# Performance work log

Hardware: AMD Instinct MI355X
Metric: run time of the kernel (lower is better)

Reference implementation:

```python
import jax, jax.numpy as jnp
import numpy as np

B, L, M, H = 4096, 512, 17, 17  # batch, seq_len, num_features, latent_dim


def setup_inputs() -> dict:
    key = jax.random.key(0)
    ks = jax.random.split(key, 5)
    s = 1.0 / np.sqrt(H)  # torch nn.LSTM init scale
    x = jax.random.normal(ks[0], (B, L, M), dtype=jnp.float32)
    W_ih = jax.random.uniform(ks[1], (4 * H, M), dtype=jnp.float32, minval=-s, maxval=s)
    W_hh = jax.random.uniform(ks[2], (4 * H, H), dtype=jnp.float32, minval=-s, maxval=s)
    b_ih = jax.random.uniform(ks[3], (4 * H,), dtype=jnp.float32, minval=-s, maxval=s)
    b_hh = jax.random.uniform(ks[4], (4 * H,), dtype=jnp.float32, minval=-s, maxval=s)
    return {"x": x, "W_ih": W_ih, "W_hh": W_hh, "b_ih": b_ih, "b_hh": b_hh}


def _lstm(x, W_ih, W_hh, b_ih, b_hh):
    # Precompute input projections for all timesteps in one GEMM: (B,L,4H)
    xW = jnp.einsum('blm,gm->blg', x, W_ih) + b_ih + b_hh
    xW_t = jnp.swapaxes(xW, 0, 1)  # (L,B,4H) for scan over time
    W_hh_T = W_hh.T  # (H,4H)

    def step(carry, xw_t):
        h, c = carry
        gates = xw_t + h @ W_hh_T  # (B,4H)
        i, f, g, o = jnp.split(gates, 4, axis=-1)  # torch gate order: i,f,g,o
        i = jax.nn.sigmoid(i)
        f = jax.nn.sigmoid(f)
        g = jnp.tanh(g)
        o = jax.nn.sigmoid(o)
        c_new = f * c + i * g
        h_new = o * jnp.tanh(c_new)
        return (h_new, c_new), h_new

    h0 = jnp.zeros((x.shape[0], W_hh.shape[1]), dtype=x.dtype)
    c0 = jnp.zeros_like(h0)
    (h_f, c_f), hs = jax.lax.scan(step, (h0, c0), xW_t)
    out = jnp.swapaxes(hs, 0, 1)  # (B,L,H)
    return out, h_f, c_f


def reference(x, W_ih, W_hh, b_ih, b_hh):
    out, h_f, c_f = _lstm(x, W_ih, W_hh, b_ih, b_hh)
    # match torch return: out, (h,c) with leading num_layers dim, and x
    return out, (h_f[None], c_f[None]), x
```

## Files before the change

kernel.cpp:

```cpp
#include <hip/hip_runtime.h>
#include <hip/hip_bf16.h>


namespace {
constexpr int B_TOT = 4096;
constexpr int L_SEQ = 512;
constexpr int NF    = 17;
constexpr int BS    = 16;
constexpr int TPB   = 320;
constexpr int TC    = 32;
constexpr int NCHUNK = L_SEQ / TC;
constexpr int KPAD  = 24;
constexpr int F4_PER_ROW   = TC * NF / 4;
constexpr int F4_PER_CHUNK = BS * F4_PER_ROW;
constexpr int PF_MAX = (F4_PER_CHUNK + TPB - 1) / TPB;

constexpr int OUT_H = B_TOT * L_SEQ * NF;
constexpr int OUT_C = OUT_H + B_TOT * NF;
constexpr int OUT_X = OUT_C + B_TOT * NF;
}

typedef __attribute__((ext_vector_type(8))) short bf16x8;
typedef __attribute__((ext_vector_type(4))) float f32x4;

__device__ __forceinline__ unsigned short f2bf(float f) {
  union { float f; unsigned int u; } v; v.f = f;
  unsigned int r = v.u + 0x7fff + ((v.u >> 16) & 1);
  return (unsigned short)(r >> 16);
}
__device__ __forceinline__ float sigm(float x) {
  return __builtin_amdgcn_rcpf(1.f + __expf(-x));
}
__device__ __forceinline__ float tanh_fast(float x) {
  float e = __expf(2.f * x);
  return 1.f - 2.f * __builtin_amdgcn_rcpf(e + 1.f);
}

__global__ void __launch_bounds__(TPB) lstm_kernel(
    const float* __restrict__ x, const float* __restrict__ W_ih,
    const float* __restrict__ W_hh, const float* __restrict__ b_ih,
    const float* __restrict__ b_hh, float* __restrict__ out)
{
  __shared__ __align__(16) unsigned short x_s[2][TC][BS][KPAD];
  __shared__ __align__(16) unsigned short h_s[2][BS][KPAD];
  __shared__ __align__(16) unsigned short w0_s[80][32];
  __shared__ __align__(16) unsigned short w1_s[80][32];
  __shared__ __align__(16) float bias_s[80];
  __shared__ __align__(16) unsigned short zero16[8];

  const int tid  = threadIdx.x;
  const int lane = tid & 63;
  const int T    = tid >> 6;
  const int bb   = lane & 15;
  const int q    = lane >> 4;
  const int b0   = blockIdx.x * BS;

  f32x4 pf[PF_MAX];
  #pragma unroll
  for (int i = 0; i < PF_MAX; ++i) {
    int u = tid + TPB * i;
    if (u < F4_PER_CHUNK) {
      int row = u / F4_PER_ROW, off = u % F4_PER_ROW;
      pf[i] = *(const f32x4*)(x + ((b0 + row) * L_SEQ) * NF + off * 4);
    }
  }

  {
    unsigned int* p = (unsigned int*)&x_s[0][0][0][0];
    for (int u = tid; u < (int)(sizeof(x_s) / 4); u += TPB) p[u] = 0;
    unsigned int* ph = (unsigned int*)&h_s[0][0][0];
    for (int u = tid; u < (int)(sizeof(h_s) / 4); u += TPB) ph[u] = 0;
    if (tid < 4) ((unsigned int*)zero16)[tid] = 0;
  }
  for (int u = tid; u < 80 * 32; u += TPB) {
    int r = u >> 5, k = u & 31;
    unsigned short v0 = 0, v1 = 0;
    int j = -1, ty = 0;
    if (r < 64)      { j = r >> 2; ty = r & 3; }
    else if (r < 68) { j = 16;     ty = r - 64; }
    if (j >= 0 && k < NF) {
      int g = ty * NF + j;
      v0 = f2bf(W_ih[g * NF + k]);
      v1 = f2bf(W_hh[g * NF + k]);
    }
    w0_s[r][k] = v0; w1_s[r][k] = v1;
  }
  for (int u = tid; u < 80; u += TPB) {
    float bv = 0.f; int j = -1, ty = 0;
    if (u < 64)      { j = u >> 2; ty = u & 3; }
    else if (u < 68) { j = 16;     ty = u - 64; }
    if (j >= 0) { int g = ty * NF + j; bv = b_ih[g] + b_hh[g]; }
    bias_s[u] = bv;
  }
  __syncthreads();

  auto stage = [&](int cn) {
    #pragma unroll
    for (int i = 0; i < PF_MAX; ++i) {
      int u = tid + TPB * i;
      if (u < F4_PER_CHUNK) {
        int row = u / F4_PER_ROW, off = u % F4_PER_ROW;
        int gidx = ((b0 + row) * L_SEQ + cn * TC) * NF + off * 4;
        *(f32x4*)(out + OUT_X + gidx) = pf[i];
        int p = off * 4, tl = p / NF, m = p - tl * NF;
        #pragma unroll
        for (int e = 0; e < 4; ++e) {
          x_s[cn & 1][tl][row][m] = f2bf(pf[i][e]);
          if (++m == NF) { m = 0; ++tl; }
        }
      }
    }
  };
  auto prefetch = [&](int cn) {
    #pragma unroll
    for (int i = 0; i < PF_MAX; ++i) {
      int u = tid + TPB * i;
      if (u < F4_PER_CHUNK) {
        int row = u / F4_PER_ROW, off = u % F4_PER_ROW;
        pf[i] = *(const f32x4*)(x + ((b0 + row) * L_SEQ + cn * TC) * NF + off * 4);
      }
    }
  };

  stage(0);
  prefetch(1);

  const bf16x8 a0 = *(const bf16x8*)&w0_s[16 * T + bb][q * 8];
  const bf16x8 a1 = *(const bf16x8*)&w1_s[16 * T + bb][q * 8];
  const f32x4 bias4 = *(const f32x4*)&bias_s[16 * T + q * 4];

  const int j = 4 * T + q;
  const bool active = (T < 4) || (q == 0);
  const int jj = (j > 16) ? 16 : j;

  const unsigned short* xbuf[2] = {
    (q == 3) ? zero16 : &x_s[0][0][bb][q * 8],
    (q == 3) ? zero16 : &x_s[1][0][bb][q * 8] };
  const int xstep = (q == 3) ? 0 : BS * KPAD;
  const unsigned short* hr[2] = {
    (q == 3) ? zero16 : &h_s[0][bb][q * 8],
    (q == 3) ? zero16 : &h_s[1][bb][q * 8] };
  unsigned short* hw[2] = { &h_s[1][bb][jj], &h_s[0][bb][jj] };

  float c_st = 0.f, h_last = 0.f;
  float* outp = out + (b0 + bb) * L_SEQ * NF + jj;

  for (int c = 0; c < NCHUNK; ++c) {
    const unsigned short* xp = xbuf[c & 1];
    for (int tt = 0; tt < TC; ++tt) {
      const int t = c * TC + tt;
      __syncthreads();
      bf16x8 bx = *(const bf16x8*)xp;
      bf16x8 bh = *(const bf16x8*)hr[t & 1];
      xp += xstep;
      f32x4 acc = __builtin_amdgcn_mfma_f32_16x16x32_bf16(a0, bx, bias4, 0, 0, 0);
      acc       = __builtin_amdgcn_mfma_f32_16x16x32_bf16(a1, bh, acc,   0, 0, 0);
      if (active) {
        float gi = sigm(acc[0]);
        float gf = sigm(acc[1]);
        float gg = tanh_fast(acc[2]);
        float go = sigm(acc[3]);
        c_st  = gf * c_st + gi * gg;
        h_last = go * tanh_fast(c_st);
        *hw[t & 1] = f2bf(h_last);
        outp[0] = h_last;
        outp += NF;
      }
    }
    if (c + 1 < NCHUNK) {
      stage(c + 1);
      if (c + 2 < NCHUNK) prefetch(c + 2);
    }
  }

  if (active) {
    out[OUT_H + (b0 + bb) * NF + j] = h_last;
    out[OUT_C + (b0 + bb) * NF + j] = c_st;
  }
}

extern "C" void kernel_launch(void* const* d_in, const int* in_sizes, int n_in,
                              void* d_out, int out_size, void* d_ws, size_t ws_size,
                              hipStream_t stream) {
  (void)in_sizes; (void)n_in; (void)out_size; (void)d_ws; (void)ws_size;
  const float* x    = (const float*)d_in[0];
  const float* W_ih = (const float*)d_in[1];
  const float* W_hh = (const float*)d_in[2];
  const float* b_ih = (const float*)d_in[3];
  const float* b_hh = (const float*)d_in[4];
  float* out = (float*)d_out;
  hipLaunchKernelGGL(lstm_kernel, dim3(B_TOT / BS), dim3(TPB), 0, stream,
                     x, W_ih, W_hh, b_ih, b_hh, out);
}
```

Baseline: 497.8 us.

## Rewrite LSTM kernel with 4 waves, register weights and per-step x staging

Cuts the block from 5 to 4 wavefronts: wave 3 computes the extra 17th hidden unit with a second pair of MFMAs. Weights and biases are loaded straight into registers instead of going through shared memory. x is streamed per timestep by wave 0 through a 4-slot register ring and a small LDS ring, replacing the chunked 32-step staging. The h buffer uses a padded, swizzled layout to avoid bank conflicts, and the barrier is a hand-written lgkmcnt wait plus s_barrier. This aims to shorten each serial step's barrier and LDS latency, but wave 3 now does twice the work and wave 0 takes on the global loads, which may make them the critical path.

```diff
diff --git a/kernel.cpp b/kernel.cpp
--- a/kernel.cpp
+++ b/kernel.cpp
@@ -1,181 +1,184 @@
 #include <hip/hip_runtime.h>
-#include <hip/hip_bf16.h>
+#include <string.h>
 
 
+typedef __attribute__((ext_vector_type(8))) short bf16x8;
+typedef __attribute__((ext_vector_type(4))) float f32x4;
+typedef __attribute__((ext_vector_type(4))) int i32x4;
+
 namespace {
-constexpr int B_TOT = 4096;
-constexpr int L_SEQ = 512;
-constexpr int NF    = 17;
-constexpr int BS    = 16;
-constexpr int TPB   = 320;
-constexpr int TC    = 32;
-constexpr int NCHUNK = L_SEQ / TC;
-constexpr int KPAD  = 24;
-constexpr int F4_PER_ROW   = TC * NF / 4;
-constexpr int F4_PER_CHUNK = BS * F4_PER_ROW;
-constexpr int PF_MAX = (F4_PER_CHUNK + TPB - 1) / TPB;
-
+constexpr int B_TOT = 4096, L_SEQ = 512, NF = 17;
 constexpr int OUT_H = B_TOT * L_SEQ * NF;
 constexpr int OUT_C = OUT_H + B_TOT * NF;
 constexpr int OUT_X = OUT_C + B_TOT * NF;
 }
 
-typedef __attribute__((ext_vector_type(8))) short bf16x8;
-typedef __attribute__((ext_vector_type(4))) float f32x4;
-
-__device__ __forceinline__ unsigned short f2bf(float f) {
-  union { float f; unsigned int u; } v; v.f = f;
-  unsigned int r = v.u + 0x7fff + ((v.u >> 16) & 1);
-  return (unsigned short)(r >> 16);
+__device__ __forceinline__ float sigm(float v) {
+  return __builtin_amdgcn_rcpf(1.f + __expf(-v));
 }
-__device__ __forceinline__ float sigm(float x) {
-  return __builtin_amdgcn_rcpf(1.f + __expf(-x));
-}
-__device__ __forceinline__ float tanh_fast(float x) {
-  float e = __expf(2.f * x);
+__device__ __forceinline__ float tanh_f(float v) {
+  float e = __expf(2.f * v);
   return 1.f - 2.f * __builtin_amdgcn_rcpf(e + 1.f);
 }
+__device__ __forceinline__ unsigned pack_bf(float a, float b) {
+  return ((__float_as_uint(a) + 0x8000u) >> 16) | ((__float_as_uint(b) + 0x8000u) & 0xffff0000u);
+}
+__device__ __forceinline__ unsigned short bf1(float a) {
+  return (unsigned short)((__float_as_uint(a) + 0x8000u) >> 16);
+}
 
-__global__ void __launch_bounds__(TPB) lstm_kernel(
+__global__ void __launch_bounds__(256) lstm_kernel(
     const float* __restrict__ x, const float* __restrict__ W_ih,
     const float* __restrict__ W_hh, const float* __restrict__ b_ih,
     const float* __restrict__ b_hh, float* __restrict__ out)
 {
-  __shared__ __align__(16) unsigned short x_s[2][TC][BS][KPAD];
-  __shared__ __align__(16) unsigned short h_s[2][BS][KPAD];
-  __shared__ __align__(16) unsigned short w0_s[80][32];
-  __shared__ __align__(16) unsigned short w1_s[80][32];
-  __shared__ __align__(16) float bias_s[80];
-  __shared__ __align__(16) unsigned short zero16[8];
+  __shared__ unsigned hx[2][4][65];
+  __shared__ unsigned xs[4][4][64];
 
   const int tid  = threadIdx.x;
   const int lane = tid & 63;
-  const int T    = tid >> 6;
+  const int w    = tid >> 6;
   const int bb   = lane & 15;
   const int q    = lane >> 4;
-  const int b0   = blockIdx.x * BS;
+  const int b0   = blockIdx.x * 16;
 
-  f32x4 pf[PF_MAX];
+  for (int u = tid; u < 2 * 4 * 65; u += 256) ((unsigned*)hx)[u] = 0;
+
+  bf16x8 a0[2], a1[2]; f32x4 bias[2];
   #pragma unroll
-  for (int i = 0; i < PF_MAX; ++i) {
-    int u = tid + TPB * i;
-    if (u < F4_PER_CHUNK) {
-      int row = u / F4_PER_ROW, off = u % F4_PER_ROW;
-      pf[i] = *(const f32x4*)(x + ((b0 + row) * L_SEQ) * NF + off * 4);
+  for (int tt = 0; tt < 2; ++tt) {
+    const int T = tt ? 4 : w;
+    unsigned d0[4], d1[4];
+    const int R = 16 * T + bb, j = R >> 2, ty = R & 3;
+    const bool vr = (j <= 16);
+    #pragma unroll
+    for (int u = 0; u < 4; ++u) {
+      const int k0 = 8 * q + u, k1 = k0 + 4;
+      float wa0 = (vr && k0 < NF) ? W_ih[(ty * NF + j) * NF + k0] : 0.f;
+      float wa1 = (vr && k1 < NF) ? W_ih[(ty * NF + j) * NF + k1] : 0.f;
+      float wb0 = (vr && k0 < NF) ? W_hh[(ty * NF + j) * NF + k0] : 0.f;
+      float wb1 = (vr && k1 < NF) ? W_hh[(ty * NF + j) * NF + k1] : 0.f;
+      d0[u] = pack_bf(wa0, wa1);
+      d1[u] = pack_bf(wb0, wb1);
+    }
+    a0[tt] = __builtin_bit_cast(bf16x8, i32x4{(int)d0[0], (int)d0[1], (int)d0[2], (int)d0[3]});
+    a1[tt] = __builtin_bit_cast(bf16x8, i32x4{(int)d1[0], (int)d1[1], (int)d1[2], (int)d1[3]});
+    f32x4 bv;
+    #pragma unroll
+    for (int r = 0; r < 4; ++r) {
+      const int Rc = 16 * T + 4 * q + r, jc = Rc >> 2, tyc = Rc & 3;
+      bv[r] = (jc <= 16) ? (b_ih[tyc * NF + jc] + b_hh[tyc * NF + jc]) : 0.f;
+    }
+    bias[tt] = bv;
+  }
+
+  float xb[4][8];
+  const int xoff = (b0 + bb) * L_SEQ * NF + 8 * q;
+
+  auto load_x = [&](int slot, int t) {
+    const float* p = x + xoff + t * NF;
+    if (q < 2) {
+      memcpy(&xb[slot][0], p, 16);
+      memcpy(&xb[slot][4], p + 4, 16);
+    } else if (q == 2) {
+      xb[slot][0] = p[0];
+      #pragma unroll
+      for (int e = 1; e < 8; ++e) xb[slot][e] = 0.f;
+    } else {
+      #pragma unroll
+      for (int e = 0; e < 8; ++e) xb[slot][e] = 0.f;
+    }
+  };
+  auto stage_x = [&](int t, int slot) {
+    #pragma unroll
+    for (int d = 0; d < 4; ++d)
+      xs[t & 3][d][lane] = pack_bf(xb[slot][d], xb[slot][d + 4]);
+    float* po = out + OUT_X + xoff + t * NF;
+    if (q < 2) {
+      memcpy(po, &xb[slot][0], 16);
+      memcpy(po + 4, &xb[slot][4], 16);
+    } else if (q == 2) {
+      po[0] = xb[slot][0];
+    }
+  };
+
+  if (w == 0) {
+    #pragma unroll
+    for (int k = 0; k < 4; ++k) load_x(k, k);
+    stage_x(0, 0);
+  }
+  __syncthreads();
+
+  unsigned short* hw0[2]; unsigned short* hw1[2];
+  const unsigned* hr[2];
+  #pragma unroll
+  for (int bf = 0; bf < 2; ++bf) {
+    unsigned* p0 = &((unsigned*)hx)[bf * 260 + q * 65 + bb * 4 + (((w >> 1) + bb) & 3)];
+    hw0[bf] = (unsigned short*)p0 + (w & 1);
+    unsigned* p1 = &((unsigned*)hx)[bf * 260 + bb * 4 + ((2 + bb) & 3)];
+    hw1[bf] = (unsigned short*)p1;
+    hr[bf] = &((unsigned*)hx)[bf * 260 + bb * 4 + ((q + bb) & 3)];
+  }
+
+  float c0 = 0.f, c1 = 0.f, hA = 0.f, hB = 0.f;
+  float* op0 = out + (b0 + bb) * L_SEQ * NF + (4 * w + q);
+  float* op1 = out + (b0 + bb) * L_SEQ * NF + 16;
+
+  for (int tb = 0; tb < L_SEQ; tb += 4) {
+    #pragma unroll
+    for (int k = 0; k < 4; ++k) {
+      const int t = tb + k;
+      unsigned bhd[4], bxd[4];
+      const unsigned* hrb = hr[t & 1];
+      #pragma unroll
+      for (int u = 0; u < 4; ++u) bhd[u] = hrb[u * 65];
+      #pragma unroll
+      for (int d = 0; d < 4; ++d) bxd[d] = ((const unsigned*)xs)[(t & 3) * 256 + d * 64 + lane];
+      bf16x8 bh = __builtin_bit_cast(bf16x8, i32x4{(int)bhd[0], (int)bhd[1], (int)bhd[2], (int)bhd[3]});
+      bf16x8 bx = __builtin_bit_cast(bf16x8, i32x4{(int)bxd[0], (int)bxd[1], (int)bxd[2], (int)bxd[3]});
+
+      f32x4 acc0 = __builtin_amdgcn_mfma_f32_16x16x32_bf16(a0[0], bx, bias[0], 0, 0, 0);
+      acc0       = __builtin_amdgcn_mfma_f32_16x16x32_bf16(a1[0], bh, acc0,    0, 0, 0);
+      f32x4 acc1;
+      if (w == 3) {
+        acc1 = __builtin_amdgcn_mfma_f32_16x16x32_bf16(a0[1], bx, bias[1], 0, 0, 0);
+        acc1 = __builtin_amdgcn_mfma_f32_16x16x32_bf16(a1[1], bh, acc1,    0, 0, 0);
+      }
+
+      {
+        float gi = sigm(acc0[0]), gf = sigm(acc0[1]);
+        float gg = tanh_f(acc0[2]), go = sigm(acc0[3]);
+        c0 = gf * c0 + gi * gg;
+        hA = go * tanh_f(c0);
+        *hw0[(t + 1) & 1] = bf1(hA);
+        op0[t * NF] = hA;
+      }
+      if (w == 3) {
+        float gi = sigm(acc1[0]), gf = sigm(acc1[1]);
+        float gg = tanh_f(acc1[2]), go = sigm(acc1[3]);
+        c1 = gf * c1 + gi * gg;
+        hB = go * tanh_f(c1);
+        if (q == 0) {
+          *hw1[(t + 1) & 1] = bf1(hB);
+          op1[t * NF] = hB;
+        }
+      }
+      if (w == 0) {
+        if (t + 1 < L_SEQ) stage_x(t + 1, (t + 1) & 3);
+        if (t + 4 < L_SEQ) load_x(t & 3, t + 4);
+      }
+      asm volatile("s_waitcnt lgkmcnt(0)\n\ts_barrier" ::: "memory");
     }
   }
 
   {
-    unsigned int* p = (unsigned int*)&x_s[0][0][0][0];
-    for (int u = tid; u < (int)(sizeof(x_s) / 4); u += TPB) p[u] = 0;
-    unsigned int* ph = (unsigned int*)&h_s[0][0][0];
-    for (int u = tid; u < (int)(sizeof(h_s) / 4); u += TPB) ph[u] = 0;
-    if (tid < 4) ((unsigned int*)zero16)[tid] = 0;
-  }
-  for (int u = tid; u < 80 * 32; u += TPB) {
-    int r = u >> 5, k = u & 31;
-    unsigned short v0 = 0, v1 = 0;
-    int j = -1, ty = 0;
-    if (r < 64)      { j = r >> 2; ty = r & 3; }
-    else if (r < 68) { j = 16;     ty = r - 64; }
-    if (j >= 0 && k < NF) {
-      int g = ty * NF + j;
-      v0 = f2bf(W_ih[g * NF + k]);
-      v1 = f2bf(W_hh[g * NF + k]);
+    const int jf = 4 * w + q;
+    out[OUT_H + (b0 + bb) * NF + jf] = hA;
+    out[OUT_C + (b0 + bb) * NF + jf] = c0;
+    if (w == 3 && q == 0) {
+      out[OUT_H + (b0 + bb) * NF + 16] = hB;
+      out[OUT_C + (b0 + bb) * NF + 16] = c1;
     }
-    w0_s[r][k] = v0; w1_s[r][k] = v1;
-  }
-  for (int u = tid; u < 80; u += TPB) {
-    float bv = 0.f; int j = -1, ty = 0;
-    if (u < 64)      { j = u >> 2; ty = u & 3; }
-    else if (u < 68) { j = 16;     ty = u - 64; }
-    if (j >= 0) { int g = ty * NF + j; bv = b_ih[g] + b_hh[g]; }
-    bias_s[u] = bv;
-  }
-  __syncthreads();
-
-  auto stage = [&](int cn) {
-    #pragma unroll
-    for (int i = 0; i < PF_MAX; ++i) {
-      int u = tid + TPB * i;
-      if (u < F4_PER_CHUNK) {
-        int row = u / F4_PER_ROW, off = u % F4_PER_ROW;
-        int gidx = ((b0 + row) * L_SEQ + cn * TC) * NF + off * 4;
-        *(f32x4*)(out + OUT_X + gidx) = pf[i];
-        int p = off * 4, tl = p / NF, m = p - tl * NF;
-        #pragma unroll
-        for (int e = 0; e < 4; ++e) {
-          x_s[cn & 1][tl][row][m] = f2bf(pf[i][e]);
-          if (++m == NF) { m = 0; ++tl; }
-        }
-      }
-    }
-  };
-  auto prefetch = [&](int cn) {
-    #pragma unroll
-    for (int i = 0; i < PF_MAX; ++i) {
-      int u = tid + TPB * i;
-      if (u < F4_PER_CHUNK) {
-        int row = u / F4_PER_ROW, off = u % F4_PER_ROW;
-        pf[i] = *(const f32x4*)(x + ((b0 + row) * L_SEQ + cn * TC) * NF + off * 4);
-      }
-    }
-  };
-
-  stage(0);
-  prefetch(1);
-
-  const bf16x8 a0 = *(const bf16x8*)&w0_s[16 * T + bb][q * 8];
-  const bf16x8 a1 = *(const bf16x8*)&w1_s[16 * T + bb][q * 8];
-  const f32x4 bias4 = *(const f32x4*)&bias_s[16 * T + q * 4];
-
-  const int j = 4 * T + q;
-  const bool active = (T < 4) || (q == 0);
-  const int jj = (j > 16) ? 16 : j;
-
-  const unsigned short* xbuf[2] = {
-    (q == 3) ? zero16 : &x_s[0][0][bb][q * 8],
-    (q == 3) ? zero16 : &x_s[1][0][bb][q * 8] };
-  const int xstep = (q == 3) ? 0 : BS * KPAD;
-  const unsigned short* hr[2] = {
-    (q == 3) ? zero16 : &h_s[0][bb][q * 8],
-    (q == 3) ? zero16 : &h_s[1][bb][q * 8] };
-  unsigned short* hw[2] = { &h_s[1][bb][jj], &h_s[0][bb][jj] };
-
-  float c_st = 0.f, h_last = 0.f;
-  float* outp = out + (b0 + bb) * L_SEQ * NF + jj;
-
-  for (int c = 0; c < NCHUNK; ++c) {
-    const unsigned short* xp = xbuf[c & 1];
-    for (int tt = 0; tt < TC; ++tt) {
-      const int t = c * TC + tt;
-      __syncthreads();
-      bf16x8 bx = *(const bf16x8*)xp;
-      bf16x8 bh = *(const bf16x8*)hr[t & 1];
-      xp += xstep;
-      f32x4 acc = __builtin_amdgcn_mfma_f32_16x16x32_bf16(a0, bx, bias4, 0, 0, 0);
-      acc       = __builtin_amdgcn_mfma_f32_16x16x32_bf16(a1, bh, acc,   0, 0, 0);
-      if (active) {
-        float gi = sigm(acc[0]);
-        float gf = sigm(acc[1]);
-        float gg = tanh_fast(acc[2]);
-        float go = sigm(acc[3]);
-        c_st  = gf * c_st + gi * gg;
-        h_last = go * tanh_fast(c_st);
-        *hw[t & 1] = f2bf(h_last);
-        outp[0] = h_last;
-        outp += NF;
-      }
-    }
-    if (c + 1 < NCHUNK) {
-      stage(c + 1);
-      if (c + 2 < NCHUNK) prefetch(c + 2);
-    }
-  }
-
-  if (active) {
-    out[OUT_H + (b0 + bb) * NF + j] = h_last;
-    out[OUT_C + (b0 + bb) * NF + j] = c_st;
   }
 }
 
@@ -189,6 +192,6 @@
   const float* b_ih = (const float*)d_in[3];
   const float* b_hh = (const float*)d_in[4];
   float* out = (float*)d_out;
-  hipLaunchKernelGGL(lstm_kernel, dim3(B_TOT / BS), dim3(TPB), 0, stream,
+  hipLaunchKernelGGL(lstm_kernel, dim3(B_TOT / 16), dim3(256), 0, stream,
                      x, W_ih, W_hh, b_ih, b_hh, out);
 }
```

Measured after the change: 1.041 ms. 2.09x slower.
